# Performance work log

Measured on AMD Instinct MI355X. Metric: run time of the kernel, lower is better.

## Reference

```python
import jax, jax.numpy as jnp
import numpy as np

N_NODES = 150000  # n_users + n_items
N_EDGES = 2400000
D = 128
LEAKY_SLOPE = 0.2  # tf.nn.leaky_relu default alpha
L2_EPS = 1e-12     # tf.math.l2_normalize epsilon


def setup_inputs() -> dict:
    key = jax.random.key(0)
    ks = jax.random.split(key, 8)
    edge_row = jax.random.randint(ks[0], (N_EDGES,), 0, N_NODES, dtype=jnp.int32)
    edge_col = jax.random.randint(ks[1], (N_EDGES,), 0, N_NODES, dtype=jnp.int32)
    edge_val = jax.random.uniform(ks[2], (N_EDGES,), dtype=jnp.float32)
    ego_embeddings = jax.random.normal(ks[3], (N_NODES, D), dtype=jnp.float32)
    w_gc = jax.random.normal(ks[4], (D, D), dtype=jnp.float32) * 0.05
    b_gc = jax.random.normal(ks[5], (D,), dtype=jnp.float32) * 0.05
    w_bi = jax.random.normal(ks[6], (D, D), dtype=jnp.float32) * 0.05
    b_bi = jax.random.normal(ks[7], (D,), dtype=jnp.float32) * 0.05
    return {"edge_row": edge_row, "edge_col": edge_col, "edge_val": edge_val,
            "ego_embeddings": ego_embeddings,
            "w_gc": w_gc, "b_gc": b_gc, "w_bi": w_bi, "b_bi": b_bi}


def reference(edge_row, edge_col, edge_val, ego_embeddings, w_gc, b_gc, w_bi, b_bi):
    # Sparse A @ ego  (concat over n_fold row-blocks == full SpMM)
    msgs = edge_val[:, None] * ego_embeddings[edge_col]          # [E, D]
    side = jax.ops.segment_sum(msgs, edge_row, num_segments=N_NODES)  # [N, D]
    # dual dense transform + leaky_relu
    sum_emb = jax.nn.leaky_relu(side @ w_gc + b_gc, negative_slope=LEAKY_SLOPE)
    bi_emb = jax.nn.leaky_relu((ego_embeddings * side) @ w_bi + b_bi,
                               negative_slope=LEAKY_SLOPE)
    ego = sum_emb + bi_emb
    # dropout rate = 1 - mess_dropout = 0 -> identity (deterministic)
    # tf.math.l2_normalize(axis=1)
    sq = jnp.sum(ego * ego, axis=1, keepdims=True)
    norm_emb = ego * jax.lax.rsqrt(jnp.maximum(sq, L2_EPS))
    return norm_emb
```

## Files before the change

### kernel.cpp

```cpp
#include <hip/hip_runtime.h>
#include <hip/hip_bf16.h>

constexpr int N_NODES = 150000;
constexpr int N_EDGES = 2400000;
constexpr int D       = 128;
constexpr float LEAKY = 0.2f;
constexpr float L2EPS = 1e-12f;

constexpr int NB_SCAN = (N_NODES + 255) / 256;

constexpr int RB_LOG = 9;
constexpr int RB     = 1 << RB_LOG;
constexpr int NBK    = (N_NODES + RB - 1) >> RB_LOG;
constexpr int EPT_A  = 32;
constexpr int EPB_A  = 256 * EPT_A;

typedef short  short8  __attribute__((ext_vector_type(8)));
typedef short  short4v __attribute__((ext_vector_type(4)));
typedef float  f32x4   __attribute__((ext_vector_type(4)));

static __device__ __forceinline__ short f2bf(float x) {
  __hip_bfloat16 h = __float2bfloat16(x);
  return *reinterpret_cast<short*>(&h);
}

__global__ __launch_bounds__(256) void hist_kernel(
    const int* __restrict__ erow, int* __restrict__ cnt) {
  int base = blockIdx.x * 2048 + threadIdx.x;
  #pragma unroll
  for (int k = 0; k < 8; ++k) {
    int e = base + k * 256;
    if (e < N_EDGES) atomicAdd(&cnt[erow[e]], 1);
  }
}

__global__ __launch_bounds__(256) void scan_block_sums(
    const int* __restrict__ cnt, int* __restrict__ bsums) {
  __shared__ int s[256];
  int i = blockIdx.x * 256 + threadIdx.x;
  s[threadIdx.x] = (i < N_NODES) ? cnt[i] : 0;
  __syncthreads();
  for (int off = 128; off > 0; off >>= 1) {
    if (threadIdx.x < off) s[threadIdx.x] += s[threadIdx.x + off];
    __syncthreads();
  }
  if (threadIdx.x == 0) bsums[blockIdx.x] = s[0];
}

__global__ __launch_bounds__(1024) void scan_partials(int* __restrict__ bsums) {
  __shared__ int s[1024];
  int v = (threadIdx.x < NB_SCAN) ? bsums[threadIdx.x] : 0;
  s[threadIdx.x] = v;
  __syncthreads();
  for (int off = 1; off < 1024; off <<= 1) {
    int t = (threadIdx.x >= off) ? s[threadIdx.x - off] : 0;
    __syncthreads();
    s[threadIdx.x] += t;
    __syncthreads();
  }
  if (threadIdx.x < NB_SCAN) bsums[threadIdx.x] = s[threadIdx.x] - v;
}

__global__ __launch_bounds__(256) void scan_final(
    const int* __restrict__ cnt, const int* __restrict__ bsums,
    int* __restrict__ offs, int* __restrict__ cursor,
    int* __restrict__ bcur) {
  __shared__ int s[256];
  int i = blockIdx.x * 256 + threadIdx.x;
  int v = (i < N_NODES) ? cnt[i] : 0;
  s[threadIdx.x] = v;
  __syncthreads();
  for (int off = 1; off < 256; off <<= 1) {
    int t = (threadIdx.x >= off) ? s[threadIdx.x - off] : 0;
    __syncthreads();
    s[threadIdx.x] += t;
    __syncthreads();
  }
  if (i < N_NODES) {
    int excl = s[threadIdx.x] - v + bsums[blockIdx.x];
    offs[i]   = excl;
    cursor[i] = excl;
    if ((i & (RB - 1)) == 0) bcur[i >> RB_LOG] = excl;
  }
  if (i == 0) offs[N_NODES] = N_EDGES;
}

__global__ __launch_bounds__(256) void bucket_scatter_kernel(
    const int*   __restrict__ erow,
    const int*   __restrict__ ecol,
    const float* __restrict__ eval,
    int*         __restrict__ bcur,
    int2*        __restrict__ stage) {
  __shared__ int h[NBK];
  __shared__ int basea[NBK];
  const int t = threadIdx.x;
  const long long e0 = (long long)blockIdx.x * EPB_A;

  for (int i = t; i < NBK; i += 256) h[i] = 0;
  __syncthreads();

  int rows[EPT_A];
  #pragma unroll
  for (int k = 0; k < EPT_A; ++k) {
    long long e = e0 + k * 256 + t;
    int r = -1;
    if (e < N_EDGES) { r = erow[e]; atomicAdd(&h[r >> RB_LOG], 1); }
    rows[k] = r;
  }
  __syncthreads();

  for (int b = t; b < NBK; b += 256) {
    int c = h[b];
    basea[b] = c ? atomicAdd(&bcur[b], c) : 0;
    h[b] = 0;
  }
  __syncthreads();

  #pragma unroll
  for (int k = 0; k < EPT_A; ++k) {
    int r = rows[k];
    if (r >= 0) {
      long long e = e0 + k * 256 + t;
      int bkt  = r >> RB_LOG;
      int rank = atomicAdd(&h[bkt], 1);
      int pos  = basea[bkt] + rank;
      int pack = ecol[e] | ((r & (RB - 1)) << 18);
      stage[pos] = make_int2(pack, __float_as_int(eval[e]));
    }
  }
}

__global__ __launch_bounds__(256) void bucket_permute_kernel(
    const int*  __restrict__ offs,
    const int2* __restrict__ stage,
    int2*       __restrict__ ev) {
  __shared__ int cur[RB];
  const int t    = threadIdx.x;
  const int row0 = blockIdx.x << RB_LOG;

  for (int i = t; i < RB; i += 256) {
    int r = row0 + i;
    cur[i] = (r < N_NODES) ? offs[r] : N_EDGES;
  }
  __syncthreads();

  const int w0 = offs[row0];
  const int w1 = offs[min(row0 + RB, N_NODES)];
  for (int i = w0 + t; i < w1; i += 256) {
    int2 e = stage[i];
    int rl  = (e.x >> 18) & (RB - 1);
    int pos = atomicAdd(&cur[rl], 1);
    ev[pos] = make_int2(e.x & 0x3FFFF, e.y);
  }
}

__global__ __launch_bounds__(256) void bin_kernel(
    const int*   __restrict__ erow,
    const int*   __restrict__ ecol,
    const float* __restrict__ eval,
    int*         __restrict__ cursor,
    int2*        __restrict__ sorted_ev) {
  int base = blockIdx.x * 1024 + threadIdx.x;
  int e0 = base, e1 = base + 256, e2 = base + 512, e3 = base + 768;
  int r0 = (e0 < N_EDGES) ? erow[e0] : 0;
  int r1 = (e1 < N_EDGES) ? erow[e1] : 0;
  int r2 = (e2 < N_EDGES) ? erow[e2] : 0;
  int r3 = (e3 < N_EDGES) ? erow[e3] : 0;
  int p0 = (e0 < N_EDGES) ? atomicAdd(&cursor[r0], 1) : 0;
  int p1 = (e1 < N_EDGES) ? atomicAdd(&cursor[r1], 1) : 0;
  int p2 = (e2 < N_EDGES) ? atomicAdd(&cursor[r2], 1) : 0;
  int p3 = (e3 < N_EDGES) ? atomicAdd(&cursor[r3], 1) : 0;
  if (e0 < N_EDGES) sorted_ev[p0] = make_int2(ecol[e0], __float_as_int(eval[e0]));
  if (e1 < N_EDGES) sorted_ev[p1] = make_int2(ecol[e1], __float_as_int(eval[e1]));
  if (e2 < N_EDGES) sorted_ev[p2] = make_int2(ecol[e2], __float_as_int(eval[e2]));
  if (e3 < N_EDGES) sorted_ev[p3] = make_int2(ecol[e3], __float_as_int(eval[e3]));
}

__global__ __launch_bounds__(256) void conv_ego_kernel(
    const float* __restrict__ ego, short* __restrict__ ebf) {
  int i = blockIdx.x * 256 + threadIdx.x;
  constexpr int TOTAL = N_NODES * D / 4;
  if (i < TOTAL) {
    float4 v = ((const float4*)ego)[i];
    short4v p;
    p[0] = f2bf(v.x); p[1] = f2bf(v.y); p[2] = f2bf(v.z); p[3] = f2bf(v.w);
    ((short4v*)ebf)[i] = p;
  }
}

__global__ __launch_bounds__(128) void prep_weights_kernel(
    const float* __restrict__ wg, const float* __restrict__ wb,
    short* __restrict__ wtg, short* __restrict__ wtb) {
  int n = blockIdx.x;
  int k = threadIdx.x;
  wtg[n * D + k] = f2bf(wg[k * D + n]);
  wtb[n * D + k] = f2bf(wb[k * D + n]);
}

__global__ __launch_bounds__(256) void spmm_bf16_kernel(
    const int*   __restrict__ offs,
    const int2*  __restrict__ ev,
    const short* __restrict__ ebf,
    float*       __restrict__ side) {
  const int t = threadIdx.x;
  const int g = t >> 4;
  const int l = t & 15;
  const int row = blockIdx.x * 16 + g;

  const int s0 = offs[row], s1 = offs[row + 1];
  float a0 = 0.f, a1 = 0.f, a2 = 0.f, a3 = 0.f;
  float a4 = 0.f, a5 = 0.f, a6 = 0.f, a7 = 0.f;

  auto accum = [&](int2 e) {
    uint4 u = *(const uint4*)(ebf + (size_t)e.x * D + l * 8);
    float v = __int_as_float(e.y);
    a0 = fmaf(v, __uint_as_float(u.x << 16), a0);
    a1 = fmaf(v, __uint_as_float(u.x & 0xffff0000u), a1);
    a2 = fmaf(v, __uint_as_float(u.y << 16), a2);
    a3 = fmaf(v, __uint_as_float(u.y & 0xffff0000u), a3);
    a4 = fmaf(v, __uint_as_float(u.z << 16), a4);
    a5 = fmaf(v, __uint_as_float(u.z & 0xffff0000u), a5);
    a6 = fmaf(v, __uint_as_float(u.w << 16), a6);
    a7 = fmaf(v, __uint_as_float(u.w & 0xffff0000u), a7);
  };

  int i = s0;
  const int n4 = s0 + ((s1 - s0) & ~3);
  for (; i < n4; i += 4) {
    int2 e0 = ev[i], e1 = ev[i + 1], e2 = ev[i + 2], e3 = ev[i + 3];
    accum(e0); accum(e1); accum(e2); accum(e3);
  }
  for (; i < s1; ++i) accum(ev[i]);

  float* dst = side + (size_t)row * D + l * 8;
  *(float4*)(dst)     = make_float4(a0, a1, a2, a3);
  *(float4*)(dst + 4) = make_float4(a4, a5, a6, a7);
}

__global__ __launch_bounds__(256) void spmm_kernel(
    const int*  __restrict__ offs,
    const int2* __restrict__ ev,
    const float* __restrict__ ego,
    float*       __restrict__ side) {
  const int t = threadIdx.x;
  const int g = t >> 5;
  const int l = t & 31;
  const int row = blockIdx.x * 8 + g;
  if (row >= N_NODES) return;
  const int s0 = offs[row], s1 = offs[row + 1];
  float ax = 0.f, ay = 0.f, az = 0.f, aw = 0.f;
  int i = s0;
  const int n4 = s0 + ((s1 - s0) & ~3);
  for (; i < n4; i += 4) {
    int2 e0 = ev[i], e1 = ev[i + 1], e2 = ev[i + 2], e3 = ev[i + 3];
    float4 g0 = *(const float4*)(ego + (size_t)e0.x * D + 4 * l);
    float4 g1 = *(const float4*)(ego + (size_t)e1.x * D + 4 * l);
    float4 g2 = *(const float4*)(ego + (size_t)e2.x * D + 4 * l);
    float4 g3 = *(const float4*)(ego + (size_t)e3.x * D + 4 * l);
    float v0 = __int_as_float(e0.y), v1 = __int_as_float(e1.y);
    float v2 = __int_as_float(e2.y), v3 = __int_as_float(e3.y);
    ax = fmaf(v0, g0.x, ax); ay = fmaf(v0, g0.y, ay);
    az = fmaf(v0, g0.z, az); aw = fmaf(v0, g0.w, aw);
    ax = fmaf(v1, g1.x, ax); ay = fmaf(v1, g1.y, ay);
    az = fmaf(v1, g1.z, az); aw = fmaf(v1, g1.w, aw);
    ax = fmaf(v2, g2.x, ax); ay = fmaf(v2, g2.y, ay);
    az = fmaf(v2, g2.z, az); aw = fmaf(v2, g2.w, aw);
    ax = fmaf(v3, g3.x, ax); ay = fmaf(v3, g3.y, ay);
    az = fmaf(v3, g3.z, az); aw = fmaf(v3, g3.w, aw);
  }
  for (; i < s1; ++i) {
    int2 e = ev[i];
    float4 gg = *(const float4*)(ego + (size_t)e.x * D + 4 * l);
    float v = __int_as_float(e.y);
    ax = fmaf(v, gg.x, ax); ay = fmaf(v, gg.y, ay);
    az = fmaf(v, gg.z, az); aw = fmaf(v, gg.w, aw);
  }
  *(float4*)(side + (size_t)row * D + 4 * l) = make_float4(ax, ay, az, aw);
}

__global__ __launch_bounds__(256) void transform_mfma_kernel(
    const float* __restrict__ side,
    const float* __restrict__ ego,
    const short* __restrict__ wtg,
    const short* __restrict__ wtb,
    const float* __restrict__ b_gc,
    const float* __restrict__ b_bi,
    float*       __restrict__ out) {
  __shared__ short sA[16][136];
  __shared__ short sP[16][136];
  __shared__ float sO[16][132];
  __shared__ float sInv[16];

  const int t    = threadIdx.x;
  const int w    = t >> 6;
  const int l    = t & 63;
  const int base = blockIdx.x * 16;

  #pragma unroll
  for (int k = 0; k < 2; ++k) {
    int f  = k * 256 + t;
    int r  = f >> 5;
    int c4 = (f & 31) * 4;
    float4 sv = *(const float4*)(side + (size_t)(base + r) * D + c4);
    float4 ev = *(const float4*)(ego  + (size_t)(base + r) * D + c4);
    short4v pa, pp;
    pa[0] = f2bf(sv.x); pa[1] = f2bf(sv.y); pa[2] = f2bf(sv.z); pa[3] = f2bf(sv.w);
    pp[0] = f2bf(sv.x * ev.x); pp[1] = f2bf(sv.y * ev.y);
    pp[2] = f2bf(sv.z * ev.z); pp[3] = f2bf(sv.w * ev.w);
    *(short4v*)&sA[r][c4] = pa;
    *(short4v*)&sP[r][c4] = pp;
  }
  __syncthreads();

  f32x4 accg[2] = {{0.f, 0.f, 0.f, 0.f}, {0.f, 0.f, 0.f, 0.f}};
  f32x4 accb[2] = {{0.f, 0.f, 0.f, 0.f}, {0.f, 0.f, 0.f, 0.f}};

  const int arow = l & 15;
  const int koff = (l >> 4) * 8;
  const int nb   = w * 32;

  #pragma unroll
  for (int ks = 0; ks < 4; ++ks) {
    const int k0 = ks * 32 + koff;
    short8 a_s = *(const short8*)&sA[arow][k0];
    short8 a_p = *(const short8*)&sP[arow][k0];
    #pragma unroll
    for (int ct = 0; ct < 2; ++ct) {
      const int n = nb + ct * 16 + arow;
      short8 bgf = *(const short8*)(wtg + (size_t)n * D + k0);
      short8 bbf = *(const short8*)(wtb + (size_t)n * D + k0);
      accg[ct] = __builtin_amdgcn_mfma_f32_16x16x32_bf16(a_s, bgf, accg[ct], 0, 0, 0);
      accb[ct] = __builtin_amdgcn_mfma_f32_16x16x32_bf16(a_p, bbf, accb[ct], 0, 0, 0);
    }
  }

  #pragma unroll
  for (int ct = 0; ct < 2; ++ct) {
    const int col = nb + ct * 16 + arow;
    const float bg = b_gc[col];
    const float bb = b_bi[col];
    #pragma unroll
    for (int j = 0; j < 4; ++j) {
      const int r = (l >> 4) * 4 + j;
      float x1 = accg[ct][j] + bg; x1 = (x1 > 0.f) ? x1 : LEAKY * x1;
      float x2 = accb[ct][j] + bb; x2 = (x2 > 0.f) ? x2 : LEAKY * x2;
      sO[r][col] = x1 + x2;
    }
  }
  __syncthreads();

  {
    const int r = t >> 4, c16 = t & 15;
    float sum = 0.f;
    #pragma unroll
    for (int i = 0; i < 8; ++i) {
      float v = sO[r][c16 * 8 + i];
      sum = fmaf(v, v, sum);
    }
    #pragma unroll
    for (int off = 8; off > 0; off >>= 1) sum += __shfl_down(sum, off, 16);
    if (c16 == 0) sInv[r] = rsqrtf(fmaxf(sum, L2EPS));
  }
  __syncthreads();

  #pragma unroll
  for (int k = 0; k < 2; ++k) {
    int f  = k * 256 + t;
    int r  = f >> 5;
    int c4 = (f & 31) * 4;
    float inv = sInv[r];
    float4 v = *(const float4*)&sO[r][c4];
    v.x *= inv; v.y *= inv; v.z *= inv; v.w *= inv;
    *(float4*)(out + (size_t)(base + r) * D + c4) = v;
  }
}

__global__ __launch_bounds__(256) void scatter_kernel(
    const int*   __restrict__ erow,
    const int*   __restrict__ ecol,
    const float* __restrict__ eval,
    const float* __restrict__ ego,
    float*       __restrict__ side) {
  long long t = (long long)blockIdx.x * blockDim.x + threadIdx.x;
  int e = (int)(t >> 5);
  if (e >= N_EDGES) return;
  int c = (int)(t & 31);
  int r  = erow[e];
  int cl = ecol[e];
  float v = eval[e];
  const float4* src = (const float4*)(ego + (long long)cl * D);
  float4 m = src[c];
  float* dst = side + (long long)r * D + c * 4;
  atomicAdd(dst + 0, v * m.x);
  atomicAdd(dst + 1, v * m.y);
  atomicAdd(dst + 2, v * m.z);
  atomicAdd(dst + 3, v * m.w);
}

__global__ __launch_bounds__(128) void transform_f32_kernel(
    const float* __restrict__ side,
    const float* __restrict__ ego,
    const float* __restrict__ w_gc,
    const float* __restrict__ b_gc,
    const float* __restrict__ w_bi,
    const float* __restrict__ b_bi,
    float*       __restrict__ out) {
  constexpr int RPB = 16;
  __shared__ float s_side[RPB][D];
  __shared__ float s_prod[RPB][D];
  __shared__ float s_part[RPB][2];
  const int j    = threadIdx.x;
  const int base = blockIdx.x * RPB;
  #pragma unroll
  for (int r = 0; r < RPB; ++r) {
    int node = base + r;
    float s = 0.f, e = 0.f;
    if (node < N_NODES) {
      s = side[(long long)node * D + j];
      e = ego [(long long)node * D + j];
    }
    s_side[r][j] = s;
    s_prod[r][j] = e * s;
  }
  __syncthreads();
  float acc_gc[RPB], acc_bi[RPB];
  #pragma unroll
  for (int r = 0; r < RPB; ++r) { acc_gc[r] = 0.f; acc_bi[r] = 0.f; }
  for (int k = 0; k < D; ++k) {
    float wg = w_gc[k * D + j];
    float wb = w_bi[k * D + j];
    #pragma unroll
    for (int r = 0; r < RPB; ++r) {
      acc_gc[r] = fmaf(s_side[r][k], wg, acc_gc[r]);
      acc_bi[r] = fmaf(s_prod[r][k], wb, acc_bi[r]);
    }
  }
  const float bg = b_gc[j];
  const float bb = b_bi[j];
  #pragma unroll
  for (int r = 0; r < RPB; ++r) {
    float x1 = acc_gc[r] + bg; x1 = (x1 > 0.f) ? x1 : LEAKY * x1;
    float x2 = acc_bi[r] + bb; x2 = (x2 > 0.f) ? x2 : LEAKY * x2;
    acc_gc[r] = x1 + x2;
  }
  const int lane = j & 63;
  const int wv   = j >> 6;
  #pragma unroll
  for (int r = 0; r < RPB; ++r) {
    float sq = acc_gc[r] * acc_gc[r];
    #pragma unroll
    for (int off = 32; off > 0; off >>= 1) sq += __shfl_down(sq, off, 64);
    if (lane == 0) s_part[r][wv] = sq;
  }
  __syncthreads();
  #pragma unroll
  for (int r = 0; r < RPB; ++r) {
    int node = base + r;
    if (node < N_NODES) {
      float tot = s_part[r][0] + s_part[r][1];
      float inv = rsqrtf(fmaxf(tot, L2EPS));
      out[(long long)node * D + j] = acc_gc[r] * inv;
    }
  }
}

extern "C" void kernel_launch(void* const* d_in, const int* in_sizes, int n_in,
                              void* d_out, int out_size, void* d_ws, size_t ws_size,
                              hipStream_t stream) {
  const int*   erow = (const int*)  d_in[0];
  const int*   ecol = (const int*)  d_in[1];
  const float* eval = (const float*)d_in[2];
  const float* ego  = (const float*)d_in[3];
  const float* w_gc = (const float*)d_in[4];
  const float* b_gc = (const float*)d_in[5];
  const float* w_bi = (const float*)d_in[6];
  const float* b_bi = (const float*)d_in[7];
  float* out = (float*)d_out;

  auto align256 = [](size_t x) { return (x + 255) & ~(size_t)255; };
  size_t off_cnt    = 0;
  size_t off_offs   = align256(off_cnt    + (size_t)N_NODES * 4);
  size_t off_cursor = align256(off_offs   + (size_t)(N_NODES + 1) * 4);
  size_t off_bsums  = align256(off_cursor + (size_t)N_NODES * 4);
  size_t off_bcur   = align256(off_bsums  + 1024 * 4);
  size_t off_wtg    = align256(off_bcur   + (size_t)NBK * 4);
  size_t off_wtb    = align256(off_wtg    + (size_t)D * D * 2);
  size_t off_ev     = align256(off_wtb    + (size_t)D * D * 2);
  size_t off_ebf    = align256(off_ev     + (size_t)N_EDGES * 8);
  size_t ws_mid     = off_ebf;
  size_t ws_sort    = off_ebf + (size_t)N_EDGES * 8;
  size_t ws_full    = off_ebf + (size_t)N_NODES * D * 2;

  if (ws_size >= ws_mid) {
    char* ws = (char*)d_ws;
    int*   cnt    = (int*)  (ws + off_cnt);
    int*   offs   = (int*)  (ws + off_offs);
    int*   cursor = (int*)  (ws + off_cursor);
    int*   bsums  = (int*)  (ws + off_bsums);
    int*   bcur   = (int*)  (ws + off_bcur);
    short* wtg    = (short*)(ws + off_wtg);
    short* wtb    = (short*)(ws + off_wtb);
    int2*  ev     = (int2*) (ws + off_ev);
    short* ebf    = (short*)(ws + off_ebf);
    int2*  stage  = (int2*) (ws + off_ebf);

    float* side = out;

    hipMemsetAsync(cnt, 0, (size_t)N_NODES * 4, stream);

    hist_kernel<<<(N_EDGES + 2047) / 2048, 256, 0, stream>>>(erow, cnt);
    scan_block_sums<<<NB_SCAN, 256, 0, stream>>>(cnt, bsums);
    scan_partials<<<1, 1024, 0, stream>>>(bsums);
    scan_final<<<NB_SCAN, 256, 0, stream>>>(cnt, bsums, offs, cursor, bcur);

    bool bucketed = (ws_size >= ws_sort);
    if (bucketed) {
      bucket_scatter_kernel<<<(N_EDGES + EPB_A - 1) / EPB_A, 256, 0, stream>>>(
          erow, ecol, eval, bcur, stage);
      bucket_permute_kernel<<<NBK, 256, 0, stream>>>(offs, stage, ev);
    } else {
      bin_kernel<<<(N_EDGES + 1023) / 1024, 256, 0, stream>>>(
          erow, ecol, eval, cursor, ev);
    }
    prep_weights_kernel<<<D, D, 0, stream>>>(w_gc, w_bi, wtg, wtb);

    if (ws_size >= ws_full) {
      conv_ego_kernel<<<(N_NODES * D / 4 + 255) / 256, 256, 0, stream>>>(ego, ebf);
      spmm_bf16_kernel<<<N_NODES / 16, 256, 0, stream>>>(offs, ev, ebf, side);
    } else {
      spmm_kernel<<<(N_NODES + 7) / 8, 256, 0, stream>>>(offs, ev, ego, side);
    }
    transform_mfma_kernel<<<N_NODES / 16, 256, 0, stream>>>(
        side, ego, wtg, wtb, b_gc, b_bi, out);
  } else {
    float* side = out;
    hipMemsetAsync(side, 0, (size_t)N_NODES * D * 4, stream);
    long long total = (long long)N_EDGES * 32;
    int grid = (int)((total + 255) / 256);
    scatter_kernel<<<grid, 256, 0, stream>>>(erow, ecol, eval, ego, side);
    transform_f32_kernel<<<N_NODES / 16, 128, 0, stream>>>(
        side, ego, w_gc, b_gc, w_bi, b_bi, out);
  }
}
```

Before: 511.2 us.

## Replace per-row histogram and scan with bucket-level histogram plus in-block row offsets

The bucketed path drops the global per-row histogram (global atomics on 150k counters) and its three scan kernels. In their place it computes a coarse per-bucket histogram using shared-memory atomics and scans it in a single block. Each permute block then counts rows within its bucket, runs a local scan to produce the row offsets, and writes offs itself. This removes the contended global atomics and several launches, at the cost of a second pass over the staged edges in the permute kernel. The code assumes RB equals twice the block size, and bbase must hold NBK+1 entries in the bsums space.

```diff
diff --git a/kernel.cpp b/kernel.cpp
--- a/kernel.cpp
+++ b/kernel.cpp
@@ -24,6 +24,49 @@
   return *reinterpret_cast<short*>(&h);
 }
 
+__global__ __launch_bounds__(256) void bucket_hist_kernel(
+    const int* __restrict__ erow, int* __restrict__ bkt_cnt) {
+  __shared__ int h[NBK];
+  const int t = threadIdx.x;
+  for (int i = t; i < NBK; i += 256) h[i] = 0;
+  __syncthreads();
+  const long long e0 = (long long)blockIdx.x * EPB_A;
+  #pragma unroll
+  for (int k = 0; k < EPT_A; ++k) {
+    long long e = e0 + k * 256 + t;
+    if (e < N_EDGES) atomicAdd(&h[erow[e] >> RB_LOG], 1);
+  }
+  __syncthreads();
+  for (int i = t; i < NBK; i += 256) {
+    int c = h[i];
+    if (c) atomicAdd(&bkt_cnt[i], c);
+  }
+}
+
+__global__ __launch_bounds__(512) void bucket_scan_kernel(
+    const int* __restrict__ bkt_cnt,
+    int* __restrict__ bbase,
+    int* __restrict__ bcur,
+    int* __restrict__ offs) {
+  __shared__ int s[512];
+  const int t = threadIdx.x;
+  int v = (t < NBK) ? bkt_cnt[t] : 0;
+  s[t] = v;
+  __syncthreads();
+  for (int off = 1; off < 512; off <<= 1) {
+    int tmp = (t >= off) ? s[t - off] : 0;
+    __syncthreads();
+    s[t] += tmp;
+    __syncthreads();
+  }
+  if (t < NBK) {
+    int excl = s[t] - v;
+    bbase[t] = excl;
+    bcur[t]  = excl;
+  }
+  if (t == 0) { bbase[NBK] = N_EDGES; offs[N_NODES] = N_EDGES; }
+}
+
 __global__ __launch_bounds__(256) void hist_kernel(
     const int* __restrict__ erow, int* __restrict__ cnt) {
   int base = blockIdx.x * 2048 + threadIdx.x;
@@ -63,8 +106,7 @@
 
 __global__ __launch_bounds__(256) void scan_final(
     const int* __restrict__ cnt, const int* __restrict__ bsums,
-    int* __restrict__ offs, int* __restrict__ cursor,
-    int* __restrict__ bcur) {
+    int* __restrict__ offs, int* __restrict__ cursor) {
   __shared__ int s[256];
   int i = blockIdx.x * 256 + threadIdx.x;
   int v = (i < N_NODES) ? cnt[i] : 0;
@@ -80,7 +122,6 @@
     int excl = s[threadIdx.x] - v + bsums[blockIdx.x];
     offs[i]   = excl;
     cursor[i] = excl;
-    if ((i & (RB - 1)) == 0) bcur[i >> RB_LOG] = excl;
   }
   if (i == 0) offs[N_NODES] = N_EDGES;
 }
@@ -131,25 +172,51 @@
 }
 
 __global__ __launch_bounds__(256) void bucket_permute_kernel(
-    const int*  __restrict__ offs,
+    const int*  __restrict__ bbase,
     const int2* __restrict__ stage,
-    int2*       __restrict__ ev) {
-  __shared__ int cur[RB];
+    int2*       __restrict__ ev,
+    int*        __restrict__ offs) {
+  __shared__ int cnt[RB];
+  __shared__ int s[256];
   const int t    = threadIdx.x;
-  const int row0 = blockIdx.x << RB_LOG;
-
-  for (int i = t; i < RB; i += 256) {
-    int r = row0 + i;
-    cur[i] = (r < N_NODES) ? offs[r] : N_EDGES;
-  }
-  __syncthreads();
-
-  const int w0 = offs[row0];
-  const int w1 = offs[min(row0 + RB, N_NODES)];
+  const int bkt  = blockIdx.x;
+  const int row0 = bkt << RB_LOG;
+  const int w0   = bbase[bkt];
+  const int w1   = bbase[bkt + 1];
+
+  for (int i = t; i < RB; i += 256) cnt[i] = 0;
+  __syncthreads();
+
+  for (int i = w0 + t; i < w1; i += 256) {
+    int px = ((const int*)stage)[2 * (size_t)i];
+    atomicAdd(&cnt[(px >> 18) & (RB - 1)], 1);
+  }
+  __syncthreads();
+
+  int c0 = cnt[2 * t], c1 = cnt[2 * t + 1];
+  int pairsum = c0 + c1;
+  s[t] = pairsum;
+  __syncthreads();
+  for (int off = 1; off < 256; off <<= 1) {
+    int v = (t >= off) ? s[t - off] : 0;
+    __syncthreads();
+    s[t] += v;
+    __syncthreads();
+  }
+  int pexcl = s[t] - pairsum;
+  int e0 = w0 + pexcl;
+  int e1 = e0 + c0;
+  cnt[2 * t]     = e0;
+  cnt[2 * t + 1] = e1;
+  int r0 = row0 + 2 * t;
+  if (r0 < N_NODES)     offs[r0]     = e0;
+  if (r0 + 1 < N_NODES) offs[r0 + 1] = e1;
+  __syncthreads();
+
   for (int i = w0 + t; i < w1; i += 256) {
     int2 e = stage[i];
     int rl  = (e.x >> 18) & (RB - 1);
-    int pos = atomicAdd(&cur[rl], 1);
+    int pos = atomicAdd(&cnt[rl], 1);
     ev[pos] = make_int2(e.x & 0x3FFFF, e.y);
   }
 }
@@ -506,19 +573,20 @@
 
     float* side = out;
 
-    hipMemsetAsync(cnt, 0, (size_t)N_NODES * 4, stream);
-
-    hist_kernel<<<(N_EDGES + 2047) / 2048, 256, 0, stream>>>(erow, cnt);
-    scan_block_sums<<<NB_SCAN, 256, 0, stream>>>(cnt, bsums);
-    scan_partials<<<1, 1024, 0, stream>>>(bsums);
-    scan_final<<<NB_SCAN, 256, 0, stream>>>(cnt, bsums, offs, cursor, bcur);
-
     bool bucketed = (ws_size >= ws_sort);
     if (bucketed) {
+      hipMemsetAsync(cnt, 0, (size_t)NBK * 4, stream);
+      bucket_hist_kernel<<<(N_EDGES + EPB_A - 1) / EPB_A, 256, 0, stream>>>(erow, cnt);
+      bucket_scan_kernel<<<1, 512, 0, stream>>>(cnt, bsums, bcur, offs);
       bucket_scatter_kernel<<<(N_EDGES + EPB_A - 1) / EPB_A, 256, 0, stream>>>(
           erow, ecol, eval, bcur, stage);
-      bucket_permute_kernel<<<NBK, 256, 0, stream>>>(offs, stage, ev);
+      bucket_permute_kernel<<<NBK, 256, 0, stream>>>(bsums, stage, ev, offs);
     } else {
+      hipMemsetAsync(cnt, 0, (size_t)N_NODES * 4, stream);
+      hist_kernel<<<(N_EDGES + 2047) / 2048, 256, 0, stream>>>(erow, cnt);
+      scan_block_sums<<<NB_SCAN, 256, 0, stream>>>(cnt, bsums);
+      scan_partials<<<1, 1024, 0, stream>>>(bsums);
+      scan_final<<<NB_SCAN, 256, 0, stream>>>(cnt, bsums, offs, cursor);
       bin_kernel<<<(N_EDGES + 1023) / 1024, 256, 0, stream>>>(
           erow, ecol, eval, cursor, ev);
     }
```

Measured after the change: 438.0 us. -14.3%, faster.
